# Kernel tuning notes

Hardware: AMD Instinct MI355X
Metric: run time of the kernel (lower is better)

The kernel has to match this reference:

```python
import jax, jax.numpy as jnp
import numpy as np
import math

B, S, D, H = 16, 512, 1024, 16
DH = D // H  # 64
NUM_DEG = 50
NUM_SPE = 512


def setup_inputs() -> dict:
    key = jax.random.key(0)
    ks = jax.random.split(key, 16)
    w = lambda k, shape: (jax.random.normal(k, shape, jnp.float32) * 0.02)
    return {
        "hidden_states": jax.random.normal(ks[0], (B, S, D), jnp.float32),
        "attention_mask": jnp.zeros((B, 1, 1, S), jnp.float32),
        "if_2d": 1,
        "in_degree": jax.random.randint(ks[1], (B, S), 0, NUM_DEG),
        "out_degree": jax.random.randint(ks[2], (B, S), 0, NUM_DEG),
        "spe": jax.random.randint(ks[3], (B, S, S), 0, NUM_SPE),
        "dist_3d": jax.random.normal(ks[4], (B, S), jnp.float32),
        "dist_m": jax.random.normal(ks[5], (B, S, S), jnp.float32),
        # Linear params stored as [in, out]; y = x @ W + b
        "Wq": w(ks[6], (D, D)), "bq": jnp.zeros((D,), jnp.float32),
        "Wk": w(ks[7], (D, D)), "bk": jnp.zeros((D,), jnp.float32),
        "Wv": w(ks[8], (D, D)), "bv": jnp.zeros((D,), jnp.float32),
        "W_in": w(ks[9], (NUM_DEG, D)),
        "W_out": w(ks[10], (NUM_DEG, D)),
        "W_spe": w(ks[11], (NUM_SPE, H)),
    }


def reference(hidden_states, attention_mask, if_2d, in_degree, out_degree,
              spe, dist_3d, dist_m, Wq, bq, Wk, bk, Wv, bv,
              W_in, W_out, W_spe):
    # if_2d == True branch (2D graph path). padding_idx=0 -> row 0 is zero.
    pad_mask = (jnp.arange(NUM_DEG) != 0).astype(hidden_states.dtype)[:, None]
    pos = (W_in * pad_mask)[in_degree] + (W_out * pad_mask)[out_degree]  # [B,S,D]
    bias = jnp.transpose(W_spe[spe], (0, 3, 1, 2))  # [B,S,S,H] -> [B,H,S,S]

    h = hidden_states + pos
    to_heads = lambda x: x.reshape(B, S, H, DH).transpose(0, 2, 1, 3)  # [B,H,S,DH]
    q = to_heads(h @ Wq + bq)
    k = to_heads(h @ Wk + bk)
    v = to_heads(h @ Wv + bv)

    scores = jnp.einsum('bhqd,bhkd->bhqk', q, k) / math.sqrt(DH)
    scores = scores + bias + attention_mask
    probs = jax.nn.softmax(scores, axis=-1)  # dropout p=0 (eval)
    ctx = jnp.einsum('bhqk,bhkd->bhqd', probs, v)  # [B,H,S,DH]
    ctx = ctx.transpose(0, 2, 1, 3).reshape(B, S, D)
    return ctx, probs
```

## Files before the change

kernel.cpp:

```cpp
#include <hip/hip_runtime.h>

#define Bc 16
#define Sc 512
#define Dc 1024
#define Hc 16
#define DHc 64

#define AS1 __attribute__((address_space(1)))
#define AS3 __attribute__((address_space(3)))

typedef __attribute__((ext_vector_type(8))) __bf16 bf16x8;
typedef __attribute__((ext_vector_type(4))) float f32x4;
typedef __attribute__((ext_vector_type(8))) unsigned short ushort8;

static __device__ __forceinline__ unsigned short f2bf(float f) {
  unsigned int u = __builtin_bit_cast(unsigned int, f);
  unsigned int r = (u + 0x7fffu + ((u >> 16) & 1u)) >> 16;
  return (unsigned short)r;
}
static __device__ __forceinline__ float bf2f(unsigned short u) {
  unsigned int x = ((unsigned int)u) << 16;
  return __builtin_bit_cast(float, x);
}

__global__ __launch_bounds__(256) void k_pos_add(
    const float* __restrict__ hidden, const int* __restrict__ ind,
    const int* __restrict__ outd, const float* __restrict__ Win,
    const float* __restrict__ Wout, unsigned short* __restrict__ hbf) {
  int row = blockIdx.x;
  int t = threadIdx.x;
  int id = ind[row], od = outd[row];
  float fi = (id != 0) ? 1.f : 0.f;
  float fo = (od != 0) ? 1.f : 0.f;
  float4 a = ((const float4*)(hidden + (size_t)row * Dc))[t];
  float4 x = ((const float4*)(Win + (size_t)id * Dc))[t];
  float4 y = ((const float4*)(Wout + (size_t)od * Dc))[t];
  ushort4 r;
  r.x = f2bf(a.x + fi * x.x + fo * y.x);
  r.y = f2bf(a.y + fi * x.y + fo * y.y);
  r.z = f2bf(a.z + fi * x.z + fo * y.z);
  r.w = f2bf(a.w + fi * x.w + fo * y.w);
  ((ushort4*)(hbf + (size_t)row * Dc))[t] = r;
}

__global__ __launch_bounds__(256) void k_wt(
    const float* __restrict__ Wq, const float* __restrict__ Wk,
    const float* __restrict__ Wv, unsigned short* __restrict__ Wtq,
    unsigned short* __restrict__ Wtk, unsigned short* __restrict__ Wtv) {
  const float* W = blockIdx.z == 0 ? Wq : blockIdx.z == 1 ? Wk : Wv;
  unsigned short* Wt = blockIdx.z == 0 ? Wtq : blockIdx.z == 1 ? Wtk : Wtv;
  __shared__ float tile[64][65];
  int k0 = blockIdx.y * 64, n0 = blockIdx.x * 64;
  int r = threadIdx.x >> 4, c4 = (threadIdx.x & 15) * 4;
  for (int rr = r; rr < 64; rr += 16) {
    float4 v = *(const float4*)(W + (size_t)(k0 + rr) * Dc + n0 + c4);
    tile[rr][c4 + 0] = v.x;
    tile[rr][c4 + 1] = v.y;
    tile[rr][c4 + 2] = v.z;
    tile[rr][c4 + 3] = v.w;
  }
  __syncthreads();
  for (int rr = r; rr < 64; rr += 16) {
    ushort4 o;
    o.x = f2bf(tile[c4 + 0][rr]);
    o.y = f2bf(tile[c4 + 1][rr]);
    o.z = f2bf(tile[c4 + 2][rr]);
    o.w = f2bf(tile[c4 + 3][rr]);
    *(ushort4*)(Wt + (size_t)(n0 + rr) * Dc + k0 + c4) = o;
  }
}

__global__ __launch_bounds__(256) void k_wspet(
    const float* __restrict__ Wspe, float* __restrict__ WspeT) {
  int idx = blockIdx.x * 256 + threadIdx.x;
  int h = idx >> 9, i = idx & 511;
  WspeT[idx] = Wspe[i * Hc + h];
}

__global__ __launch_bounds__(256) void k_gemm_mfma(
    const unsigned short* __restrict__ hbf,
    const unsigned short* __restrict__ Wtq, const float* __restrict__ bq,
    const unsigned short* __restrict__ Wtk, const float* __restrict__ bk,
    const unsigned short* __restrict__ Wtv, const float* __restrict__ bv,
    unsigned short* __restrict__ Qo, unsigned short* __restrict__ Ko,
    unsigned short* __restrict__ Vt) {
  int zsel = blockIdx.z;
  const unsigned short* Wt;
  const float* bias;
  if (zsel == 0) { Wt = Wtq; bias = bq; }
  else if (zsel == 1) { Wt = Wtk; bias = bk; }
  else { Wt = Wtv; bias = bv; }

  __shared__ __align__(16) unsigned short As[128 * 32];
  __shared__ __align__(16) unsigned short Bs[128 * 32];

  int tid = threadIdx.x, lane = tid & 63, wave = tid >> 6;
  int m0 = blockIdx.y * 128, n0 = blockIdx.x * 128;
  int wr = wave >> 1, wc = wave & 1;

  f32x4 acc[4][4] = {};

  int srow = lane >> 2;
  int skb = (lane & 3) * 8;
  const unsigned short* gA = hbf + (size_t)(m0 + srow) * Dc + skb;
  const unsigned short* gB = Wt + (size_t)(n0 + srow) * Dc + skb;

  int fr = lane & 15, kg = (lane >> 4) * 8;

  for (int k0 = 0; k0 < Dc; k0 += 32) {
#pragma unroll
    for (int cc = 0; cc < 2; ++cc) {
      int c = wave + cc * 4;
      __builtin_amdgcn_global_load_lds(
          (const AS1 void*)(gA + (size_t)c * 16 * Dc + k0),
          (AS3 void*)(As + c * 16 * 32), 16, 0, 0);
      __builtin_amdgcn_global_load_lds(
          (const AS1 void*)(gB + (size_t)c * 16 * Dc + k0),
          (AS3 void*)(Bs + c * 16 * 32), 16, 0, 0);
    }
    __syncthreads();

    bf16x8 af[4], bfr[4];
#pragma unroll
    for (int m = 0; m < 4; ++m)
      af[m] = *(const bf16x8*)(As + (wr * 64 + m * 16 + fr) * 32 + kg);
#pragma unroll
    for (int n = 0; n < 4; ++n)
      bfr[n] = *(const bf16x8*)(Bs + (wc * 64 + n * 16 + fr) * 32 + kg);
#pragma unroll
    for (int m = 0; m < 4; ++m)
#pragma unroll
      for (int n = 0; n < 4; ++n)
        acc[m][n] = __builtin_amdgcn_mfma_f32_16x16x32_bf16(af[m], bfr[n], acc[m][n], 0, 0, 0);
    __syncthreads();
  }

  int fq = lane >> 4;
  if (zsel < 2) {
    unsigned short* C = (zsel == 0) ? Qo : Ko;
    float scale = (zsel == 0) ? 0.125f : 1.f;
#pragma unroll
    for (int m = 0; m < 4; ++m) {
#pragma unroll
      for (int n = 0; n < 4; ++n) {
        int col = n0 + wc * 64 + n * 16 + fr;
        float bb = bias[col];
#pragma unroll
        for (int r = 0; r < 4; ++r) {
          int row = m0 + wr * 64 + m * 16 + fq * 4 + r;
          C[(size_t)row * Dc + col] = f2bf((acc[m][n][r] + bb) * scale);
        }
      }
    }
  } else {
#pragma unroll
    for (int m = 0; m < 4; ++m) {
#pragma unroll
      for (int n = 0; n < 4; ++n) {
        int col = n0 + wc * 64 + n * 16 + fr;
        int hh = col >> 6, dh = col & 63;
        float bb = bias[col];
        int row = m0 + wr * 64 + m * 16 + fq * 4;
        int bb_ = row >> 9, ss = row & 511;
        ushort4 pk;
        pk.x = f2bf(acc[m][n][0] + bb);
        pk.y = f2bf(acc[m][n][1] + bb);
        pk.z = f2bf(acc[m][n][2] + bb);
        pk.w = f2bf(acc[m][n][3] + bb);
        *(ushort4*)(Vt + ((size_t)(bb_ * Hc + hh) * DHc + dh) * Sc + ss) = pk;
      }
    }
  }
}

#define SWB 520
__global__ __launch_bounds__(256, 8) void k_attn(
    const unsigned short* __restrict__ Qb, const unsigned short* __restrict__ Kb,
    const unsigned short* __restrict__ Vt, const int* __restrict__ spe,
    const float* __restrict__ WspeT, const float* __restrict__ mask,
    float* __restrict__ probs, float* __restrict__ ctx) {
  extern __shared__ char smem[];
  unsigned short* S = (unsigned short*)smem;
  float* Wb = (float*)(smem + 16640);
  float* Rinv = (float*)(smem + 16640 + 2048);

  int tid = threadIdx.x, lane = tid & 63, w = tid >> 6;
  int fr = lane & 15, fq = lane >> 4, kg8 = fq * 8;

  int flat = blockIdx.x;
  int swz = (flat & 7) * 1024 + (flat >> 3);
  int qt = swz & 31, h = (swz >> 5) & 15, b = swz >> 9;
  int q0 = qt * 16;

  for (int i = tid; i < 512; i += 256) Wb[i] = WspeT[h * 512 + i];

  const unsigned short* qbase = Qb + (size_t)(b * Sc + q0) * Dc + h * DHc;
  bf16x8 af[2];
#pragma unroll
  for (int kk = 0; kk < 2; ++kk)
    af[kk] = *(const bf16x8*)(qbase + (size_t)fr * Dc + kk * 32 + kg8);

  const unsigned short* kptr =
      Kb + (size_t)(b * Sc + w * 16 + fr) * Dc + h * DHc;
  bf16x8 kfA0 = *(const bf16x8*)(kptr + kg8);
  bf16x8 kfA1 = *(const bf16x8*)(kptr + 32 + kg8);
#pragma unroll
  for (int it = 0; it < 8; ++it) {
    bf16x8 kfB0, kfB1;
    if (it < 7) {
      const unsigned short* np = kptr + (size_t)(it + 1) * 64 * Dc;
      kfB0 = *(const bf16x8*)(np + kg8);
      kfB1 = *(const bf16x8*)(np + 32 + kg8);
    }
    f32x4 acc = {};
    __builtin_amdgcn_s_setprio(1);
    acc = __builtin_amdgcn_mfma_f32_16x16x32_bf16(kfA0, af[0], acc, 0, 0, 0);
    acc = __builtin_amdgcn_mfma_f32_16x16x32_bf16(kfA1, af[1], acc, 0, 0, 0);
    __builtin_amdgcn_s_setprio(0);
    ushort4 pk;
    pk.x = f2bf(acc[0]); pk.y = f2bf(acc[1]);
    pk.z = f2bf(acc[2]); pk.w = f2bf(acc[3]);
    *(ushort4*)(S + fr * SWB + it * 64 + w * 16 + fq * 4) = pk;
    kfA0 = kfB0; kfA1 = kfB1;
  }
  __syncthreads();

  float ri0, ri1, ri2, ri3;
  {
    const int* spp0 = spe + (size_t)(b * Sc + q0 + w * 4) * Sc + lane * 8;
    float4 mk0 = *(const float4*)(mask + b * Sc + lane * 8);
    float4 mk1 = *(const float4*)(mask + b * Sc + lane * 8 + 4);
#pragma unroll
    for (int r4 = 0; r4 < 4; ++r4) {
      int row = w * 4 + r4;
      int4 i0 = *(const int4*)(spp0 + (size_t)r4 * Sc);
      int4 i1 = *(const int4*)(spp0 + (size_t)r4 * Sc + 4);
      ushort8 sv = *(const ushort8*)(S + row * SWB + lane * 8);
      float e0 = __expf(bf2f(sv[0]) + Wb[i0.x] + mk0.x);
      float e1 = __expf(bf2f(sv[1]) + Wb[i0.y] + mk0.y);
      float e2 = __expf(bf2f(sv[2]) + Wb[i0.z] + mk0.z);
      float e3 = __expf(bf2f(sv[3]) + Wb[i0.w] + mk0.w);
      float e4 = __expf(bf2f(sv[4]) + Wb[i1.x] + mk1.x);
      float e5 = __expf(bf2f(sv[5]) + Wb[i1.y] + mk1.y);
      float e6 = __expf(bf2f(sv[6]) + Wb[i1.z] + mk1.z);
      float e7 = __expf(bf2f(sv[7]) + Wb[i1.w] + mk1.w);
      float sum = e0 + e1 + e2 + e3 + e4 + e5 + e6 + e7;
#pragma unroll
      for (int o = 32; o; o >>= 1) sum += __shfl_xor(sum, o);
      float rinv = 1.f / sum;
      if (r4 == 0) ri0 = rinv;
      else if (r4 == 1) ri1 = rinv;
      else if (r4 == 2) ri2 = rinv;
      else ri3 = rinv;
      ushort8 ev;
      ev[0] = f2bf(e0); ev[1] = f2bf(e1); ev[2] = f2bf(e2); ev[3] = f2bf(e3);
      ev[4] = f2bf(e4); ev[5] = f2bf(e5); ev[6] = f2bf(e6); ev[7] = f2bf(e7);
      *(ushort8*)(S + row * SWB + lane * 8) = ev;
      if (lane == 0) Rinv[row] = rinv;
    }
  }
  __syncthreads();

  const unsigned short* vptr =
      Vt + ((size_t)(b * Hc + h) * DHc + w * 16 + fr) * Sc;
  float* pbase = probs + (size_t)((b * Hc + h) * Sc + q0) * Sc;
  int prow = tid >> 4, pc0 = (tid & 15) * 4;
  float prv = (fq == 0) ? ri0 : (fq == 1) ? ri1 : (fq == 2) ? ri2 : ri3;
  f32x4 pacc0 = {}, pacc1 = {};
  bf16x8 vfA0 = *(const bf16x8*)(vptr + kg8);
  bf16x8 vfA1 = *(const bf16x8*)(vptr + 32 + kg8);
  ushort4 svA = *(const ushort4*)(S + prow * SWB + pc0);
#pragma unroll
  for (int it = 0; it < 8; ++it) {
    bf16x8 vfB0, vfB1;
    ushort4 svB;
    if (it < 7) {
      vfB0 = *(const bf16x8*)(vptr + (it + 1) * 64 + kg8);
      vfB1 = *(const bf16x8*)(vptr + (it + 1) * 64 + 32 + kg8);
      svB = *(const ushort4*)(S + prow * SWB + (it + 1) * 64 + pc0);
    }
    {
      f32x4 e;
      e[0] = bf2f(svA.x) * prv; e[1] = bf2f(svA.y) * prv;
      e[2] = bf2f(svA.z) * prv; e[3] = bf2f(svA.w) * prv;
      __builtin_nontemporal_store(e, (f32x4*)(pbase + (size_t)prow * Sc + it * 64 + pc0));
    }
    bf16x8 pfr0 = *(const bf16x8*)(S + fr * SWB + it * 64 + kg8);
    bf16x8 pfr1 = *(const bf16x8*)(S + fr * SWB + it * 64 + 32 + kg8);
    __builtin_amdgcn_s_setprio(1);
    pacc0 = __builtin_amdgcn_mfma_f32_16x16x32_bf16(vfA0, pfr0, pacc0, 0, 0, 0);
    pacc1 = __builtin_amdgcn_mfma_f32_16x16x32_bf16(vfA1, pfr1, pacc1, 0, 0, 0);
    __builtin_amdgcn_s_setprio(0);
    vfA0 = vfB0; vfA1 = vfB1; svA = svB;
  }

  {
    float rv = Rinv[fr];
    f32x4 o;
    o[0] = (pacc0[0] + pacc1[0]) * rv;
    o[1] = (pacc0[1] + pacc1[1]) * rv;
    o[2] = (pacc0[2] + pacc1[2]) * rv;
    o[3] = (pacc0[3] + pacc1[3]) * rv;
    __builtin_nontemporal_store(
        o, (f32x4*)(ctx + (size_t)(b * Sc + q0 + fr) * Dc + h * DHc + w * 16 + fq * 4));
  }
}

extern "C" void kernel_launch(void* const* d_in, const int* in_sizes, int n_in,
                              void* d_out, int out_size, void* d_ws, size_t ws_size,
                              hipStream_t stream) {
  const float* hidden = (const float*)d_in[0];
  const float* amask = (const float*)d_in[1];
  const int* ind = (const int*)d_in[3];
  const int* outd = (const int*)d_in[4];
  const int* spe = (const int*)d_in[5];
  const float* Wq = (const float*)d_in[8];
  const float* bq = (const float*)d_in[9];
  const float* Wk = (const float*)d_in[10];
  const float* bk = (const float*)d_in[11];
  const float* Wv = (const float*)d_in[12];
  const float* bv = (const float*)d_in[13];
  const float* Win = (const float*)d_in[14];
  const float* Wout = (const float*)d_in[15];
  const float* Wspe = (const float*)d_in[16];

  char* ws = (char*)d_ws;
  const size_t BSD = (size_t)Bc * Sc * Dc;
  unsigned short* hbf = (unsigned short*)ws;
  unsigned short* Wtq = (unsigned short*)(ws + 16u * 1048576);
  unsigned short* Wtk = (unsigned short*)(ws + 18u * 1048576);
  unsigned short* Wtv = (unsigned short*)(ws + 20u * 1048576);
  float* WspeT = (float*)(ws + 22u * 1048576);
  unsigned short* Qb = (unsigned short*)(ws + 24u * 1048576);
  unsigned short* Kb = (unsigned short*)(ws + 40u * 1048576);
  unsigned short* Vt = (unsigned short*)(ws + 56u * 1048576);
  float* ctx = (float*)d_out;
  float* probs = (float*)d_out + BSD;

  (void)hipFuncSetAttribute((const void*)k_attn,
                            hipFuncAttributeMaxDynamicSharedMemorySize, 18752);

  k_pos_add<<<dim3(Bc * Sc), 256, 0, stream>>>(hidden, ind, outd, Win, Wout, hbf);
  k_wt<<<dim3(16, 16, 3), 256, 0, stream>>>(Wq, Wk, Wv, Wtq, Wtk, Wtv);
  k_wspet<<<dim3(32), 256, 0, stream>>>(Wspe, WspeT);
  k_gemm_mfma<<<dim3(8, 64, 3), 256, 0, stream>>>(hbf, Wtq, bq, Wtk, bk, Wtv, bv, Qb, Kb, Vt);
  k_attn<<<dim3(8192), 256, 18752, stream>>>(Qb, Kb, Vt, spe, WspeT, amask, probs, ctx);
}
```

Measured before the change: 241.9 us.

## Merge prep kernels into one launch and write probs directly from softmax registers

Three small preprocessing kernels (positional add, weight transpose, spe-table transpose) are combined into one launch that dispatches on block index, which removes two kernel launches and their gaps. In the attention kernel, normalized probabilities are now written straight from the fp32 exp values held in registers during the softmax pass. This replaces re-reading bf16 values from LDS inside the PV loop, which also gives probs full fp32 precision. The full __syncthreads is replaced by an LDS-only wait plus a barrier, so the global probs stores are not drained before the PV phase.

```diff
diff --git a/kernel.cpp b/kernel.cpp
--- a/kernel.cpp
+++ b/kernel.cpp
@@ -23,58 +23,60 @@
   return __builtin_bit_cast(float, x);
 }
 
-__global__ __launch_bounds__(256) void k_pos_add(
+__global__ __launch_bounds__(256) void k_prep(
     const float* __restrict__ hidden, const int* __restrict__ ind,
     const int* __restrict__ outd, const float* __restrict__ Win,
-    const float* __restrict__ Wout, unsigned short* __restrict__ hbf) {
-  int row = blockIdx.x;
+    const float* __restrict__ Wout, const float* __restrict__ Wq,
+    const float* __restrict__ Wk, const float* __restrict__ Wv,
+    const float* __restrict__ Wspe, unsigned short* __restrict__ hbf,
+    unsigned short* __restrict__ Wtq, unsigned short* __restrict__ Wtk,
+    unsigned short* __restrict__ Wtv, float* __restrict__ WspeT) {
+  __shared__ float tile[64][65];
+  int blk = blockIdx.x;
   int t = threadIdx.x;
-  int id = ind[row], od = outd[row];
-  float fi = (id != 0) ? 1.f : 0.f;
-  float fo = (od != 0) ? 1.f : 0.f;
-  float4 a = ((const float4*)(hidden + (size_t)row * Dc))[t];
-  float4 x = ((const float4*)(Win + (size_t)id * Dc))[t];
-  float4 y = ((const float4*)(Wout + (size_t)od * Dc))[t];
-  ushort4 r;
-  r.x = f2bf(a.x + fi * x.x + fo * y.x);
-  r.y = f2bf(a.y + fi * x.y + fo * y.y);
-  r.z = f2bf(a.z + fi * x.z + fo * y.z);
-  r.w = f2bf(a.w + fi * x.w + fo * y.w);
-  ((ushort4*)(hbf + (size_t)row * Dc))[t] = r;
-}
-
-__global__ __launch_bounds__(256) void k_wt(
-    const float* __restrict__ Wq, const float* __restrict__ Wk,
-    const float* __restrict__ Wv, unsigned short* __restrict__ Wtq,
-    unsigned short* __restrict__ Wtk, unsigned short* __restrict__ Wtv) {
-  const float* W = blockIdx.z == 0 ? Wq : blockIdx.z == 1 ? Wk : Wv;
-  unsigned short* Wt = blockIdx.z == 0 ? Wtq : blockIdx.z == 1 ? Wtk : Wtv;
-  __shared__ float tile[64][65];
-  int k0 = blockIdx.y * 64, n0 = blockIdx.x * 64;
-  int r = threadIdx.x >> 4, c4 = (threadIdx.x & 15) * 4;
-  for (int rr = r; rr < 64; rr += 16) {
-    float4 v = *(const float4*)(W + (size_t)(k0 + rr) * Dc + n0 + c4);
-    tile[rr][c4 + 0] = v.x;
-    tile[rr][c4 + 1] = v.y;
-    tile[rr][c4 + 2] = v.z;
-    tile[rr][c4 + 3] = v.w;
-  }
-  __syncthreads();
-  for (int rr = r; rr < 64; rr += 16) {
-    ushort4 o;
-    o.x = f2bf(tile[c4 + 0][rr]);
-    o.y = f2bf(tile[c4 + 1][rr]);
-    o.z = f2bf(tile[c4 + 2][rr]);
-    o.w = f2bf(tile[c4 + 3][rr]);
-    *(ushort4*)(Wt + (size_t)(n0 + rr) * Dc + k0 + c4) = o;
-  }
-}
-
-__global__ __launch_bounds__(256) void k_wspet(
-    const float* __restrict__ Wspe, float* __restrict__ WspeT) {
-  int idx = blockIdx.x * 256 + threadIdx.x;
-  int h = idx >> 9, i = idx & 511;
-  WspeT[idx] = Wspe[i * Hc + h];
+  if (blk < 8192) {
+    int row = blk;
+    int id = ind[row], od = outd[row];
+    float fi = (id != 0) ? 1.f : 0.f;
+    float fo = (od != 0) ? 1.f : 0.f;
+    float4 a = ((const float4*)(hidden + (size_t)row * Dc))[t];
+    float4 x = ((const float4*)(Win + (size_t)id * Dc))[t];
+    float4 y = ((const float4*)(Wout + (size_t)od * Dc))[t];
+    ushort4 r;
+    r.x = f2bf(a.x + fi * x.x + fo * y.x);
+    r.y = f2bf(a.y + fi * x.y + fo * y.y);
+    r.z = f2bf(a.z + fi * x.z + fo * y.z);
+    r.w = f2bf(a.w + fi * x.w + fo * y.w);
+    ((ushort4*)(hbf + (size_t)row * Dc))[t] = r;
+  } else if (blk < 8960) {
+    int f = blk - 8192;
+    int z = f >> 8, rem = f & 255;
+    int ky = rem >> 4, nx = rem & 15;
+    const float* W = z == 0 ? Wq : z == 1 ? Wk : Wv;
+    unsigned short* Wt = z == 0 ? Wtq : z == 1 ? Wtk : Wtv;
+    int k0 = ky * 64, n0 = nx * 64;
+    int r = t >> 4, c4 = (t & 15) * 4;
+    for (int rr = r; rr < 64; rr += 16) {
+      float4 v = *(const float4*)(W + (size_t)(k0 + rr) * Dc + n0 + c4);
+      tile[rr][c4 + 0] = v.x;
+      tile[rr][c4 + 1] = v.y;
+      tile[rr][c4 + 2] = v.z;
+      tile[rr][c4 + 3] = v.w;
+    }
+    __syncthreads();
+    for (int rr = r; rr < 64; rr += 16) {
+      ushort4 o;
+      o.x = f2bf(tile[c4 + 0][rr]);
+      o.y = f2bf(tile[c4 + 1][rr]);
+      o.z = f2bf(tile[c4 + 2][rr]);
+      o.w = f2bf(tile[c4 + 3][rr]);
+      *(ushort4*)(Wt + (size_t)(n0 + rr) * Dc + k0 + c4) = o;
+    }
+  } else {
+    int idx = (blk - 8960) * 256 + t;
+    int h = idx >> 9, i = idx & 511;
+    WspeT[idx] = Wspe[i * Hc + h];
+  }
 }
 
 __global__ __launch_bounds__(256) void k_gemm_mfma(
@@ -225,8 +227,8 @@
   }
   __syncthreads();
 
-  float ri0, ri1, ri2, ri3;
   {
+    float* pbase = probs + (size_t)((b * Hc + h) * Sc + q0) * Sc;
     const int* spp0 = spe + (size_t)(b * Sc + q0 + w * 4) * Sc + lane * 8;
     float4 mk0 = *(const float4*)(mask + b * Sc + lane * 8);
     float4 mk1 = *(const float4*)(mask + b * Sc + lane * 8 + 4);
@@ -244,46 +246,38 @@
       float e5 = __expf(bf2f(sv[5]) + Wb[i1.y] + mk1.y);
       float e6 = __expf(bf2f(sv[6]) + Wb[i1.z] + mk1.z);
       float e7 = __expf(bf2f(sv[7]) + Wb[i1.w] + mk1.w);
-      float sum = e0 + e1 + e2 + e3 + e4 + e5 + e6 + e7;
-#pragma unroll
-      for (int o = 32; o; o >>= 1) sum += __shfl_xor(sum, o);
-      float rinv = 1.f / sum;
-      if (r4 == 0) ri0 = rinv;
-      else if (r4 == 1) ri1 = rinv;
-      else if (r4 == 2) ri2 = rinv;
-      else ri3 = rinv;
       ushort8 ev;
       ev[0] = f2bf(e0); ev[1] = f2bf(e1); ev[2] = f2bf(e2); ev[3] = f2bf(e3);
       ev[4] = f2bf(e4); ev[5] = f2bf(e5); ev[6] = f2bf(e6); ev[7] = f2bf(e7);
       *(ushort8*)(S + row * SWB + lane * 8) = ev;
+      float sum = e0 + e1 + e2 + e3 + e4 + e5 + e6 + e7;
+#pragma unroll
+      for (int o = 32; o; o >>= 1) sum += __shfl_xor(sum, o);
+      float rinv = 1.f / sum;
+      f32x4 p0, p1;
+      p0[0] = e0 * rinv; p0[1] = e1 * rinv; p0[2] = e2 * rinv; p0[3] = e3 * rinv;
+      p1[0] = e4 * rinv; p1[1] = e5 * rinv; p1[2] = e6 * rinv; p1[3] = e7 * rinv;
+      float* pdst = pbase + (size_t)row * Sc + lane * 8;
+      __builtin_nontemporal_store(p0, (f32x4*)pdst);
+      __builtin_nontemporal_store(p1, (f32x4*)(pdst + 4));
       if (lane == 0) Rinv[row] = rinv;
     }
   }
-  __syncthreads();
+  asm volatile("s_waitcnt lgkmcnt(0)" ::: "memory");
+  __builtin_amdgcn_s_barrier();
+  __builtin_amdgcn_sched_barrier(0);
 
   const unsigned short* vptr =
       Vt + ((size_t)(b * Hc + h) * DHc + w * 16 + fr) * Sc;
-  float* pbase = probs + (size_t)((b * Hc + h) * Sc + q0) * Sc;
-  int prow = tid >> 4, pc0 = (tid & 15) * 4;
-  float prv = (fq == 0) ? ri0 : (fq == 1) ? ri1 : (fq == 2) ? ri2 : ri3;
   f32x4 pacc0 = {}, pacc1 = {};
   bf16x8 vfA0 = *(const bf16x8*)(vptr + kg8);
   bf16x8 vfA1 = *(const bf16x8*)(vptr + 32 + kg8);
-  ushort4 svA = *(const ushort4*)(S + prow * SWB + pc0);
 #pragma unroll
   for (int it = 0; it < 8; ++it) {
     bf16x8 vfB0, vfB1;
-    ushort4 svB;
     if (it < 7) {
       vfB0 = *(const bf16x8*)(vptr + (it + 1) * 64 + kg8);
       vfB1 = *(const bf16x8*)(vptr + (it + 1) * 64 + 32 + kg8);
-      svB = *(const ushort4*)(S + prow * SWB + (it + 1) * 64 + pc0);
-    }
-    {
-      f32x4 e;
-      e[0] = bf2f(svA.x) * prv; e[1] = bf2f(svA.y) * prv;
-      e[2] = bf2f(svA.z) * prv; e[3] = bf2f(svA.w) * prv;
-      __builtin_nontemporal_store(e, (f32x4*)(pbase + (size_t)prow * Sc + it * 64 + pc0));
     }
     bf16x8 pfr0 = *(const bf16x8*)(S + fr * SWB + it * 64 + kg8);
     bf16x8 pfr1 = *(const bf16x8*)(S + fr * SWB + it * 64 + 32 + kg8);
@@ -291,7 +285,7 @@
     pacc0 = __builtin_amdgcn_mfma_f32_16x16x32_bf16(vfA0, pfr0, pacc0, 0, 0, 0);
     pacc1 = __builtin_amdgcn_mfma_f32_16x16x32_bf16(vfA1, pfr1, pacc1, 0, 0, 0);
     __builtin_amdgcn_s_setprio(0);
-    vfA0 = vfB0; vfA1 = vfB1; svA = svB;
+    vfA0 = vfB0; vfA1 = vfB1;
   }
 
   {
@@ -340,9 +334,8 @@
   (void)hipFuncSetAttribute((const void*)k_attn,
                             hipFuncAttributeMaxDynamicSharedMemorySize, 18752);
 
-  k_pos_add<<<dim3(Bc * Sc), 256, 0, stream>>>(hidden, ind, outd, Win, Wout, hbf);
-  k_wt<<<dim3(16, 16, 3), 256, 0, stream>>>(Wq, Wk, Wv, Wtq, Wtk, Wtv);
-  k_wspet<<<dim3(32), 256, 0, stream>>>(Wspe, WspeT);
+  k_prep<<<dim3(8992), 256, 0, stream>>>(hidden, ind, outd, Win, Wout, Wq, Wk,
+                                         Wv, Wspe, hbf, Wtq, Wtk, Wtv, WspeT);
   k_gemm_mfma<<<dim3(8, 64, 3), 256, 0, stream>>>(hbf, Wtq, bq, Wtk, bk, Wtv, bv, Qb, Kb, Vt);
   k_attn<<<dim3(8192), 256, 18752, stream>>>(Qb, Kb, Vt, spe, WspeT, amask, probs, ctx);
 }
```

Measured after the change: 247.7 us. +2.4%, slower.
